# Kernel optimization log

Hardware: AMD Instinct MI355X
Metric: run time of the kernel (lower is better)

## Reference

```python
import jax, jax.numpy as jnp
import numpy as np

D_MODEL = 1024
H = 16
D_K = D_MODEL // H


def setup_inputs() -> dict:
    key = jax.random.key(0)
    ks = jax.random.split(key, 8)
    B, S = 2, 2048
    scale = 1.0 / np.sqrt(D_MODEL)
    return {
        "query": jax.random.normal(ks[0], (B, S, D_MODEL), dtype=jnp.float32),
        "key": jax.random.normal(ks[1], (B, S, D_MODEL), dtype=jnp.float32),
        "value": jax.random.normal(ks[2], (B, S, D_MODEL), dtype=jnp.float32),
        "mask": jnp.ones((B, 1, 1, S), dtype=jnp.int32),
        "Wq": jax.random.normal(ks[3], (D_MODEL, D_MODEL), dtype=jnp.float32) * scale,
        "Wk": jax.random.normal(ks[4], (D_MODEL, D_MODEL), dtype=jnp.float32) * scale,
        "Wv": jax.random.normal(ks[5], (D_MODEL, D_MODEL), dtype=jnp.float32) * scale,
        "Wo": jax.random.normal(ks[6], (D_MODEL, D_MODEL), dtype=jnp.float32) * scale,
    }


def reference(query, key, value, mask, Wq, Wk, Wv, Wo):
    # mask is a no-op in the original (masked_fill result discarded); dropout=0.
    B, S, _ = query.shape
    q = (query @ Wq.T).reshape(B, S, H, D_K)  # [B,S,H,Dk]
    k = (key @ Wk.T).reshape(B, S, H, D_K)
    v = (value @ Wv.T).reshape(B, S, H, D_K)
    # scores = Q K^T / sqrt(d_k)  -- NOTE: no softmax in the source module
    scores = jnp.einsum("bqhd,bkhd->bhqk", q, k) / jnp.sqrt(jnp.float32(D_K))
    out = jnp.einsum("bhqk,bkhd->bqhd", scores, v).reshape(B, S, D_MODEL)
    return out @ Wo.T
```

## Files before the change

kernel.cpp:

```cpp
#include <hip/hip_runtime.h>

#define DEV __device__ __forceinline__

typedef __attribute__((ext_vector_type(8))) short short8;
typedef __attribute__((ext_vector_type(4))) float f32x4;

DEV short f2bf(float x) {
  unsigned u = __float_as_uint(x);
  unsigned r = (u + 0x7fffu + ((u >> 16) & 1u)) >> 16;
  return (short)r;
}
DEV float bf2f(short x) {
  return __uint_as_float(((unsigned)(unsigned short)x) << 16);
}

DEV void gload_lds16(const void* g, void* l) {
  __builtin_amdgcn_global_load_lds((const __attribute__((address_space(1))) void*)g,
                                   (__attribute__((address_space(3))) void*)l, 16, 0, 0);
}

__global__ __launch_bounds__(256) void cvt_all(
    const float* __restrict__ s0, const float* __restrict__ s1,
    const float* __restrict__ s2, const float* __restrict__ s3,
    const float* __restrict__ s4, const float* __restrict__ s5,
    short* __restrict__ d0, short* __restrict__ d1, short* __restrict__ d2,
    short* __restrict__ d3, short* __restrict__ d4, short* __restrict__ d5,
    float* __restrict__ Mb) {
  int g = blockIdx.x * 256 + threadIdx.x;
  if (g >= 1966080) {
    int off = g - 1966080;
    float4 z = {0.f, 0.f, 0.f, 0.f};
    float4* p = reinterpret_cast<float4*>(Mb) + (size_t)off * 2;
    p[0] = z;
    p[1] = z;
    return;
  }
  const float* s;
  short* d;
  int off;
  if (g < 524288) { s = s0; d = d0; off = g; }
  else if (g < 1048576) { s = s1; d = d1; off = g - 524288; }
  else if (g < 1572864) { s = s2; d = d2; off = g - 1048576; }
  else {
    int w2 = g - 1572864;
    int seg = w2 >> 17;
    off = w2 & 131071;
    s = seg == 0 ? s3 : seg == 1 ? s4 : s5;
    d = seg == 0 ? d3 : seg == 1 ? d4 : d5;
  }
  const float4* p = reinterpret_cast<const float4*>(s) + (size_t)off * 2;
  float4 a = p[0], b = p[1];
  short8 o;
  o[0] = f2bf(a.x); o[1] = f2bf(a.y); o[2] = f2bf(a.z); o[3] = f2bf(a.w);
  o[4] = f2bf(b.x); o[5] = f2bf(b.y); o[6] = f2bf(b.z); o[7] = f2bf(b.w);
  *reinterpret_cast<short8*>(d + (size_t)off * 8) = o;
}

template <typename OutT>
__global__ __launch_bounds__(256, 8) void gemm64(const short* __restrict__ A,
                                                 const short* __restrict__ W,
                                                 OutT* __restrict__ C,
                                                 long strideA, long strideW, long strideC) {
  __shared__ short At[64 * 64];
  __shared__ short Bt[64 * 64];
  const int nx = gridDim.x, ny = gridDim.y;
  int flat = blockIdx.x + nx * (blockIdx.y + ny * blockIdx.z);
  int nwg = nx * ny * gridDim.z;
  int l2 = (flat & 7) * (nwg >> 3) + (flat >> 3);
  int colB = l2 % nx;
  int tmp = l2 / nx;
  int rowB = tmp % ny;
  int zB = tmp / ny;

  const short* Ab = A + (size_t)zB * strideA;
  const short* Wb = W + (size_t)zB * strideW;
  OutT* Cb = C + (size_t)zB * strideC;
  const int t = threadIdx.x;
  const int w = t >> 6;
  const int l = t & 63;
  const int lg = l >> 4, lr = l & 15;
  const int wm = w >> 1, wn = w & 1;
  const int rowBase = rowB * 64;
  const int colBase = colB * 64;

  f32x4 acc[2][2] = {};

  for (int kt = 0; kt < 16; ++kt) {
    const int k0 = kt * 64;
    __syncthreads();
#pragma unroll
    for (int i = 0; i < 2; ++i) {
      int c = w * 128 + i * 64 + l;
      int r = c >> 3, s = c & 7;
      gload_lds16(Ab + (size_t)(rowBase + r) * 1024 + k0 + ((s ^ (r & 7)) << 3),
                  At + (size_t)c * 8);
    }
#pragma unroll
    for (int i = 0; i < 2; ++i) {
      int c = w * 128 + i * 64 + l;
      int r = c >> 3, s = c & 7;
      gload_lds16(Wb + (size_t)(colBase + r) * 1024 + k0 + ((s ^ (r & 7)) << 3),
                  Bt + (size_t)c * 8);
    }
    __syncthreads();
#pragma unroll
    for (int kk = 0; kk < 2; ++kk) {
      short8 afr[2], bfr[2];
#pragma unroll
      for (int m = 0; m < 2; ++m) {
        int ar = wm * 32 + m * 16 + lr;
        int slot = (kk * 4 + lg) ^ (ar & 7);
        afr[m] = *reinterpret_cast<const short8*>(&At[ar * 64 + slot * 8]);
      }
#pragma unroll
      for (int n = 0; n < 2; ++n) {
        int br = wn * 32 + n * 16 + lr;
        int slot = (kk * 4 + lg) ^ (br & 7);
        bfr[n] = *reinterpret_cast<const short8*>(&Bt[br * 64 + slot * 8]);
      }
#pragma unroll
      for (int m = 0; m < 2; ++m)
#pragma unroll
        for (int n = 0; n < 2; ++n)
          acc[m][n] = __builtin_amdgcn_mfma_f32_16x16x32_bf16(afr[m], bfr[n], acc[m][n], 0, 0, 0);
    }
  }
#pragma unroll
  for (int m = 0; m < 2; ++m)
#pragma unroll
    for (int n = 0; n < 2; ++n) {
      int row0 = rowBase + wm * 32 + m * 16 + lg * 4;
      int col = colBase + wn * 32 + n * 16 + lr;
#pragma unroll
      for (int j = 0; j < 4; ++j) {
        float v = acc[m][n][j];
        if constexpr (sizeof(OutT) == 2)
          Cb[(size_t)(row0 + j) * 1024 + col] = (OutT)f2bf(v);
        else
          Cb[(size_t)(row0 + j) * 1024 + col] = (OutT)v;
      }
    }
}

__global__ __launch_bounds__(256) void kv_outer(const short* __restrict__ Kp,
                                                const short* __restrict__ Vp,
                                                float* __restrict__ Mb) {
  __shared__ float Ks[128][64];
  __shared__ float Vs[128][64];
  const int t = threadIdx.x;
  const int sc = blockIdx.x, h = blockIdx.y, b = blockIdx.z;
  const size_t base = ((size_t)(b * 2048 + sc * 128)) * 1024 + h * 64;
  for (int e = t; e < 128 * 64; e += 256) {
    int r = e >> 6, c = e & 63;
    size_t g = base + (size_t)r * 1024 + c;
    Ks[r][c] = bf2f(Kp[g]);
    Vs[r][c] = bf2f(Vp[g]);
  }
  __syncthreads();
  const int dp0 = (t >> 4) * 4, d0 = (t & 15) * 4;
  float acc[4][4] = {};
  for (int s = 0; s < 128; ++s) {
    float4 kv = *reinterpret_cast<const float4*>(&Ks[s][dp0]);
    float4 vv = *reinterpret_cast<const float4*>(&Vs[s][d0]);
    float ka[4] = {kv.x, kv.y, kv.z, kv.w};
    float va[4] = {vv.x, vv.y, vv.z, vv.w};
#pragma unroll
    for (int i = 0; i < 4; ++i)
#pragma unroll
      for (int j = 0; j < 4; ++j) acc[i][j] += ka[i] * va[j];
  }
  float* dst = Mb + (size_t)(b * 16 + h) * 4096;
#pragma unroll
  for (int i = 0; i < 4; ++i)
#pragma unroll
    for (int j = 0; j < 4; ++j)
      atomicAdd(&dst[(dp0 + i) * 64 + d0 + j], acc[i][j] * 0.125f);
}

__global__ __launch_bounds__(256) void make_w2t(const float* __restrict__ Mb,
                                                const float* __restrict__ Wo,
                                                short* __restrict__ W2T) {
  __shared__ float Ms[64][65];
  __shared__ float Wos[64][64];
  const int t = threadIdx.x;
  const int jc = blockIdx.x, h = blockIdx.y, b = blockIdx.z;
  const float* Msrc = Mb + (size_t)(b * 16 + h) * 4096;
  for (int e = t; e < 4096; e += 256) {
    int r = e >> 6, c = e & 63;
    Ms[r][c] = Msrc[e];
    Wos[r][c] = Wo[(size_t)(jc * 64 + r) * 1024 + h * 64 + c];
  }
  __syncthreads();
  const int j0 = (t >> 4) * 4, p0 = (t & 15) * 4;
  float acc[4][4] = {};
  for (int d = 0; d < 64; ++d) {
    float wv[4], mv[4];
#pragma unroll
    for (int i = 0; i < 4; ++i) { wv[i] = Wos[j0 + i][d]; mv[i] = Ms[p0 + i][d]; }
#pragma unroll
    for (int i = 0; i < 4; ++i)
#pragma unroll
      for (int j2 = 0; j2 < 4; ++j2) acc[i][j2] += wv[i] * mv[j2];
  }
  short* dst = W2T + (size_t)b * 1048576;
#pragma unroll
  for (int i = 0; i < 4; ++i)
#pragma unroll
    for (int j2 = 0; j2 < 4; ++j2)
      dst[(size_t)(jc * 64 + j0 + i) * 1024 + h * 64 + p0 + j2] = f2bf(acc[i][j2]);
}

extern "C" void kernel_launch(void* const* d_in, const int* in_sizes, int n_in,
                              void* d_out, int out_size, void* d_ws, size_t ws_size,
                              hipStream_t stream) {
  const float* q  = (const float*)d_in[0];
  const float* k  = (const float*)d_in[1];
  const float* v  = (const float*)d_in[2];
  const float* Wq = (const float*)d_in[4];
  const float* Wk = (const float*)d_in[5];
  const float* Wv = (const float*)d_in[6];
  const float* Wo = (const float*)d_in[7];
  float* out = (float*)d_out;
  char* ws = (char*)d_ws;

  short* qkv = (short*)(ws);
  short* qb = qkv;
  short* kb = qkv + (size_t)4194304;
  short* vb = qkv + (size_t)8388608;
  short* wb = (short*)(ws + (24l << 20));
  short* wqb = wb;
  short* wkb = wb + 1048576;
  short* wvb = wb + 2097152;
  short* Pp = (short*)(ws + (30l << 20));
  short* Qp = Pp;
  short* Kp = Pp + (size_t)4194304;
  short* Vp = Pp + (size_t)8388608;
  float* Mb  = (float*)(ws + (54l << 20));
  short* W2T = (short*)(ws + (55l << 20));

  cvt_all<<<7744, 256, 0, stream>>>(q, k, v, Wq, Wk, Wv,
                                    qb, kb, vb, wqb, wkb, wvb, Mb);

  gemm64<short><<<dim3(16, 64, 3), 256, 0, stream>>>(
      qkv, wb, Pp, 4194304l, 1048576l, 4194304l);

  kv_outer<<<dim3(16, 16, 2), 256, 0, stream>>>(Kp, Vp, Mb);

  make_w2t<<<dim3(16, 16, 2), 256, 0, stream>>>(Mb, Wo, W2T);

  gemm64<float><<<dim3(16, 32, 2), 256, 0, stream>>>(
      Qp, W2T, out, 2097152l, 1048576l, 2097152l);
}
```

Baseline: 210.2 us.

## Double-buffer LDS tiles in gemm64 to overlap global loads with MFMA

Gives the bf16 GEMM kernel two LDS buffers for A and B. The global->LDS load of the next K tile is issued before the MFMAs on the current tile run, so load latency overlaps compute. The per-thread global and LDS address offsets are also precomputed once, outside the K loop. LDS per block doubles to 32KB, which may limit how many blocks fit per CU at the requested 8-block occupancy. The correctness of the overlap relies on global_load_lds being waited on by the following barrier.

```diff
diff --git a/kernel.cpp b/kernel.cpp
--- a/kernel.cpp
+++ b/kernel.cpp
@@ -61,8 +61,8 @@
                                                  const short* __restrict__ W,
                                                  OutT* __restrict__ C,
                                                  long strideA, long strideW, long strideC) {
-  __shared__ short At[64 * 64];
-  __shared__ short Bt[64 * 64];
+  __shared__ short At[2][64 * 64];
+  __shared__ short Bt[2][64 * 64];
   const int nx = gridDim.x, ny = gridDim.y;
   int flat = blockIdx.x + nx * (blockIdx.y + ny * blockIdx.z);
   int nwg = nx * ny * gridDim.z;
@@ -83,48 +83,63 @@
   const int rowBase = rowB * 64;
   const int colBase = colB * 64;
 
+  int cC[2];
+  size_t gA[2], gB[2];
+#pragma unroll
+  for (int i = 0; i < 2; ++i) {
+    int c = w * 128 + i * 64 + l;
+    int r = c >> 3, s = c & 7;
+    cC[i] = c;
+    size_t swz = (size_t)((s ^ (r & 7)) << 3);
+    gA[i] = (size_t)(rowBase + r) * 1024 + swz;
+    gB[i] = (size_t)(colBase + r) * 1024 + swz;
+  }
+
+#define STAGE(buf, kt)                                              \
+  {                                                                 \
+    const int k0_ = (kt) * 64;                                      \
+    _Pragma("unroll") for (int i = 0; i < 2; ++i) {                 \
+      gload_lds16(Ab + gA[i] + k0_, &At[buf][cC[i] * 8]);           \
+      gload_lds16(Wb + gB[i] + k0_, &Bt[buf][cC[i] * 8]);           \
+    }                                                               \
+  }
+
+#define COMPUTE(buf)                                                          \
+  {                                                                           \
+    _Pragma("unroll") for (int kk = 0; kk < 2; ++kk) {                        \
+      short8 afr[2], bfr[2];                                                  \
+      _Pragma("unroll") for (int m = 0; m < 2; ++m) {                         \
+        int ar = wm * 32 + m * 16 + lr;                                       \
+        int slot = (kk * 4 + lg) ^ (ar & 7);                                  \
+        afr[m] = *reinterpret_cast<const short8*>(&At[buf][ar * 64 + slot * 8]); \
+      }                                                                       \
+      _Pragma("unroll") for (int n = 0; n < 2; ++n) {                         \
+        int br = wn * 32 + n * 16 + lr;                                       \
+        int slot = (kk * 4 + lg) ^ (br & 7);                                  \
+        bfr[n] = *reinterpret_cast<const short8*>(&Bt[buf][br * 64 + slot * 8]); \
+      }                                                                       \
+      _Pragma("unroll") for (int m = 0; m < 2; ++m)                           \
+          _Pragma("unroll") for (int n = 0; n < 2; ++n)                       \
+              acc[m][n] = __builtin_amdgcn_mfma_f32_16x16x32_bf16(            \
+                  afr[m], bfr[n], acc[m][n], 0, 0, 0);                        \
+    }                                                                         \
+  }
+
   f32x4 acc[2][2] = {};
 
-  for (int kt = 0; kt < 16; ++kt) {
-    const int k0 = kt * 64;
+  STAGE(0, 0);
+  __syncthreads();
+  for (int kt2 = 0; kt2 < 8; ++kt2) {
+    STAGE(1, kt2 * 2 + 1);
+    COMPUTE(0);
     __syncthreads();
-#pragma unroll
-    for (int i = 0; i < 2; ++i) {
-      int c = w * 128 + i * 64 + l;
-      int r = c >> 3, s = c & 7;
-      gload_lds16(Ab + (size_t)(rowBase + r) * 1024 + k0 + ((s ^ (r & 7)) << 3),
-                  At + (size_t)c * 8);
-    }
-#pragma unroll
-    for (int i = 0; i < 2; ++i) {
-      int c = w * 128 + i * 64 + l;
-      int r = c >> 3, s = c & 7;
-      gload_lds16(Wb + (size_t)(colBase + r) * 1024 + k0 + ((s ^ (r & 7)) << 3),
-                  Bt + (size_t)c * 8);
-    }
+    if (kt2 < 7) STAGE(0, kt2 * 2 + 2);
+    COMPUTE(1);
     __syncthreads();
-#pragma unroll
-    for (int kk = 0; kk < 2; ++kk) {
-      short8 afr[2], bfr[2];
-#pragma unroll
-      for (int m = 0; m < 2; ++m) {
-        int ar = wm * 32 + m * 16 + lr;
-        int slot = (kk * 4 + lg) ^ (ar & 7);
-        afr[m] = *reinterpret_cast<const short8*>(&At[ar * 64 + slot * 8]);
-      }
-#pragma unroll
-      for (int n = 0; n < 2; ++n) {
-        int br = wn * 32 + n * 16 + lr;
-        int slot = (kk * 4 + lg) ^ (br & 7);
-        bfr[n] = *reinterpret_cast<const short8*>(&Bt[br * 64 + slot * 8]);
-      }
-#pragma unroll
-      for (int m = 0; m < 2; ++m)
-#pragma unroll
-        for (int n = 0; n < 2; ++n)
-          acc[m][n] = __builtin_amdgcn_mfma_f32_16x16x32_bf16(afr[m], bfr[n], acc[m][n], 0, 0, 0);
-    }
-  }
+  }
+#undef STAGE
+#undef COMPUTE
+
 #pragma unroll
   for (int m = 0; m < 2; ++m)
 #pragma unroll
```

New measurement: 217.2 us. 3.4% more time.
